# Optimization experiments

Measured on AMD Instinct MI355X. Metric: run time of the kernel, lower is better.

## Reference

```python
import jax, jax.numpy as jnp
import numpy as np

N, E, D_IN, D_OUT = 50000, 600000, 128, 128
BETA, ALPHA = 0.4, 0.6


def setup_inputs() -> dict:
    key = jax.random.key(0)
    ks = jax.random.split(key, 8)
    def xavier(k, shape):
        std = (2.0 / (shape[0] + shape[1])) ** 0.5
        return jax.random.normal(k, shape, jnp.float32) * std
    x = jax.random.normal(ks[0], (N, D_IN), jnp.float32)
    edge_index = jax.random.randint(ks[1], (2, E), 0, N, jnp.int32)
    Wq = xavier(ks[2], (D_IN, D_OUT))
    Wk = xavier(ks[3], (D_IN, D_OUT))
    Wv = xavier(ks[4], (D_IN, D_IN))
    W_gcn = xavier(ks[5], (D_IN, D_IN))   # GCNConv linear weight [out, in]
    b_gcn = jnp.zeros((D_IN,), jnp.float32)
    W_lin = xavier(ks[6], (D_OUT, D_IN))  # nn.Linear weight [out, in]
    b_lin = jnp.zeros((D_OUT,), jnp.float32)
    return {"x": x, "edge_index": edge_index, "Wq": Wq, "Wk": Wk, "Wv": Wv,
            "W_gcn": W_gcn, "b_gcn": b_gcn, "W_lin": W_lin, "b_lin": b_lin}


def gcn_conv(x, edge_index, W, b):
    # PyG GCNConv default: add self-loops, symmetric deg^-1/2 normalization.
    n = x.shape[0]
    loops = jnp.arange(n, dtype=edge_index.dtype)
    src = jnp.concatenate([edge_index[0], loops])
    dst = jnp.concatenate([edge_index[1], loops])
    deg = jax.ops.segment_sum(jnp.ones_like(dst, jnp.float32), dst, num_segments=n)
    d_inv_sqrt = jax.lax.rsqrt(deg)  # deg >= 1 thanks to self-loops
    norm = d_inv_sqrt[src] * d_inv_sqrt[dst]  # [E+N]
    xw = x @ W.T                               # [N, d]
    out = jax.ops.segment_sum(xw[src] * norm[:, None], dst, num_segments=n)
    return out + b


def reference(x, edge_index, Wq, Wk, Wv, W_gcn, b_gcn, W_lin, b_lin):
    n, d_in = x.shape
    q = x @ Wq
    q_hat = q / jnp.linalg.norm(q)  # Frobenius norm
    k = x @ Wk
    k_hat = k / jnp.linalg.norm(k)
    v = x @ Wv
    # qk = q_hat @ (k_hat^T @ 1) / in_channels  -> [n]
    qk = (q_hat @ k_hat.sum(axis=0)) / d_in
    # D = diag(1 + qk); inverse of diagonal is elementwise reciprocal
    scale = 1.0 / (1.0 + qk)
    attn = v + (q_hat @ (k_hat.T @ v)) / d_in  # [n, d_in]
    Z = BETA * scale[:, None] * attn + (1.0 - BETA) * x
    gcn = gcn_conv(x, edge_index, W_gcn, b_gcn)
    # self.dropout(gcn) result is discarded in the source -> no-op
    Z_out = (1.0 - ALPHA) * Z + ALPHA * gcn
    return Z_out @ W_lin.T + b_lin
```

## Files before the change

kernel.cpp:

```cpp
#include <hip/hip_runtime.h>
#include <hip/hip_fp16.h>
#include <cstdint>
#include <cstddef>

#define D 128
#define XTS 72
typedef unsigned short u16;
typedef short bf16x8 __attribute__((ext_vector_type(8)));
typedef float f32x4 __attribute__((ext_vector_type(4)));

__device__ __forceinline__ u16 f2b(float f) {
    uint32_t u = __float_as_uint(f);
    return (u16)((u + 0x7FFFu + ((u >> 16) & 1u)) >> 16);
}
__device__ __forceinline__ float b2f(u16 b) {
    return __uint_as_float(((uint32_t)b) << 16);
}

#define SWZ(r, k) ((k) ^ (((r) & 7) << 3))

__global__ void k_prep(const float* __restrict__ Wv, const float* __restrict__ Wg,
                       const float* __restrict__ bg, const float* __restrict__ Wl,
                       const float* __restrict__ bl,
                       u16* __restrict__ Bcatb, float* __restrict__ biasout)
{
    const int b = blockIdx.x;
    const int t = threadIdx.x;
    if (b < 384) {
        const int strip = b >> 7, n = b & 127;
        float val;
        if (strip == 0) {
            float s = 0.f;
#pragma unroll 8
            for (int m = 0; m < D; ++m) s += Wv[t * D + m] * Wl[n * D + m];
            val = s;
        } else if (strip == 1) {
            val = Wl[n * D + t];
        } else {
            float s = 0.f;
#pragma unroll 8
            for (int m = 0; m < D; ++m) s += Wl[n * D + m] * Wg[m * D + t];
            val = 0.6f * s;
        }
        Bcatb[(size_t)b * D + t] = f2b(val);
    } else {
        float s = 0.f;
#pragma unroll 8
        for (int m = 0; m < D; ++m) s += bg[m] * Wl[t * D + m];
        biasout[t] = bl[t] + 0.6f * s;
    }
}

__global__ void k_init(int* __restrict__ cnt, int M)
{
    const int i = blockIdx.x * 256 + threadIdx.x;
    if (i < M) cnt[i] = 0;
}

__global__ void k_hist(const int* __restrict__ dst, int* __restrict__ cnt,
                       int* __restrict__ epos, int E)
{
    const int e = blockIdx.x * 256 + threadIdx.x;
    if (e < E) epos[e] = atomicAdd(&cnt[dst[e]], 1);
}

__global__ __launch_bounds__(1024) void k_scan1(const int* __restrict__ cnt,
                                                int* __restrict__ offs,
                                                int* __restrict__ bsum,
                                                float* __restrict__ dinv, int M)
{
    __shared__ int wsum[16];
    const int t = threadIdx.x, lane = t & 63, w = t >> 6;
    const int i = blockIdx.x * 1024 + t;
    const int v = (i < M) ? cnt[i] : 0;
    if (i < M) dinv[i] = rsqrtf((float)(v + 1));
    int s = v;
    for (int off = 1; off < 64; off <<= 1) {
        int n = __shfl_up(s, off);
        if (lane >= off) s += n;
    }
    if (lane == 63) wsum[w] = s;
    __syncthreads();
    if (w == 0) {
        int ss = (lane < 16) ? wsum[lane] : 0;
        for (int off = 1; off < 16; off <<= 1) {
            int n = __shfl_up(ss, off);
            if (lane >= off) ss += n;
        }
        if (lane < 16) wsum[lane] = ss;
    }
    __syncthreads();
    const int woff = (w == 0) ? 0 : wsum[w - 1];
    if (i < M) offs[i] = woff + s - v;
    if (t == 1023) bsum[blockIdx.x] = wsum[15];
}

__global__ void k_scanB(int* __restrict__ bsum, int nb)
{
    const int t = threadIdx.x;
    int v = (t < nb) ? bsum[t] : 0;
    int s = v;
    for (int off = 1; off < 64; off <<= 1) {
        int n = __shfl_up(s, off);
        if (t >= off) s += n;
    }
    if (t < nb) bsum[t] = s - v;
}

__global__ void k_scan2(const int* __restrict__ bsum, int* __restrict__ offs, int M)
{
    const int i = blockIdx.x * 256 + threadIdx.x;
    if (i < M) offs[i] += bsum[i >> 10];
}

__global__ void k_fill(const int* __restrict__ src, const int* __restrict__ dst,
                       const int* __restrict__ epos,
                       const float* __restrict__ dinv,
                       const int* __restrict__ offs,
                       uint32_t* __restrict__ cpk, int E)
{
    const int e = blockIdx.x * 256 + threadIdx.x;
    if (e < E) {
        const int s = src[e], d = dst[e];
        const int pos = offs[d] + epos[e];
        const float w = dinv[s] * dinv[d];
        const u16 hb = __half_as_ushort(__float2half(w));
        cpk[pos] = (uint32_t)(u16)s | ((uint32_t)hb << 16);
    }
}

__global__ __launch_bounds__(256) void k_gram(const float* __restrict__ x,
                                              u16* __restrict__ part,
                                              float* __restrict__ pcs, int M)
{
    __shared__ u16 xT[D * XTS];
    const int t = threadIdx.x;
    const int P = (int)gridDim.x;
    const int chunk = (M + P - 1) / P;
    const int rbeg = blockIdx.x * chunk;
    const int rend = min(rbeg + chunk, M);
    const int lane = t & 63, w = t >> 6;
    const int fr = lane & 15, kg = lane >> 4;

    f32x4 acc[2][8] = {};
    float csacc = 0.f;

    for (int r0 = rbeg; r0 < rend; r0 += 64) {
#pragma unroll
        for (int p = 0; p < 8; ++p) {
            const int flat = t + 256 * p;
            const int rr = flat & 63;
            const int c4 = flat >> 6;
            const int gr = r0 + rr;
            float4 v = make_float4(0.f, 0.f, 0.f, 0.f);
            if (gr < rend) v = *(const float4*)(x + (size_t)gr * D + c4 * 4);
            u16* dst = xT + (c4 * 4) * XTS + rr;
            dst[0]       = f2b(v.x);
            dst[XTS]     = f2b(v.y);
            dst[2 * XTS] = f2b(v.z);
            dst[3 * XTS] = f2b(v.w);
        }
        __syncthreads();
#pragma unroll
        for (int ks = 0; ks < 2; ++ks) {
            const int rb = ks * 32 + kg * 8;
            bf16x8 a[2], b[8];
#pragma unroll
            for (int i = 0; i < 2; ++i) {
                const int m = w * 32 + 16 * i + fr;
                a[i] = *(const bf16x8*)(xT + m * XTS + rb);
            }
#pragma unroll
            for (int j = 0; j < 8; ++j) {
                const int n = 16 * j + fr;
                b[j] = *(const bf16x8*)(xT + n * XTS + rb);
            }
#pragma unroll
            for (int i = 0; i < 2; ++i)
#pragma unroll
                for (int j = 0; j < 8; ++j)
                    acc[i][j] = __builtin_amdgcn_mfma_f32_16x16x32_bf16(a[i], b[j], acc[i][j], 0, 0, 0);
        }
        if (t < D) {
            const u16* col = xT + t * XTS;
#pragma unroll 16
            for (int r = 0; r < 64; ++r) csacc += b2f(col[r]);
        }
        __syncthreads();
    }
    u16* pp = part + (size_t)blockIdx.x * (D * D);
#pragma unroll
    for (int i = 0; i < 2; ++i)
#pragma unroll
        for (int reg = 0; reg < 4; ++reg) {
            const int m = w * 32 + 16 * i + kg * 4 + reg;
#pragma unroll
            for (int j = 0; j < 8; ++j)
                pp[(size_t)m * D + 16 * j + fr] = f2b(acc[i][j][reg]);
        }
    if (t < D) pcs[(size_t)blockIdx.x * D + t] = csacc;
}

__global__ void k_redC(const u16* __restrict__ part, float* __restrict__ Craw,
                       const float* __restrict__ pcs, float* __restrict__ csx, int P)
{
    if (blockIdx.x < 64) {
        const int e = blockIdx.x * 256 + threadIdx.x;
        float s0 = 0.f, s1 = 0.f, s2 = 0.f, s3 = 0.f,
              s4 = 0.f, s5 = 0.f, s6 = 0.f, s7 = 0.f;
        int p = 0;
        for (; p + 8 <= P; p += 8) {
            s0 += b2f(part[(size_t)(p + 0) * (D * D) + e]);
            s1 += b2f(part[(size_t)(p + 1) * (D * D) + e]);
            s2 += b2f(part[(size_t)(p + 2) * (D * D) + e]);
            s3 += b2f(part[(size_t)(p + 3) * (D * D) + e]);
            s4 += b2f(part[(size_t)(p + 4) * (D * D) + e]);
            s5 += b2f(part[(size_t)(p + 5) * (D * D) + e]);
            s6 += b2f(part[(size_t)(p + 6) * (D * D) + e]);
            s7 += b2f(part[(size_t)(p + 7) * (D * D) + e]);
        }
        for (; p < P; ++p) s0 += b2f(part[(size_t)p * (D * D) + e]);
        Craw[e] = ((s0 + s1) + (s2 + s3)) + ((s4 + s5) + (s6 + s7));
    } else {
        __shared__ float red[16][16];
        const int pb = blockIdx.x - 64;
        const int cl = threadIdx.x & 15;
        const int sl = threadIdx.x >> 4;
        const int col = pb * 16 + cl;
        float s = 0.f;
#pragma unroll 8
        for (int p = sl; p < P; p += 16) s += pcs[(size_t)p * D + col];
        red[sl][cl] = s;
        __syncthreads();
        if (sl == 0) {
            float tot = 0.f;
#pragma unroll
            for (int i = 0; i < 16; ++i) tot += red[i][cl];
            csx[col] = tot;
        }
    }
}

__device__ __forceinline__ void gemm16x64(const u16* __restrict__ A,
                                          const u16* __restrict__ B,
                                          f32x4 acc[4], int rw, int cw,
                                          int fr, int kg)
{
#pragma unroll
    for (int ks = 0; ks < 4; ++ks) {
        const int kb = ks * 32 + kg * 8;
        const int r = rw + fr;
        const bf16x8 a = *(const bf16x8*)(A + r * D + SWZ(r, kb));
#pragma unroll
        for (int j = 0; j < 4; ++j) {
            const int n = cw + 16 * j + fr;
            const bf16x8 b = *(const bf16x8*)(B + n * D + SWZ(n, kb));
            acc[j] = __builtin_amdgcn_mfma_f32_16x16x32_bf16(a, b, acc[j], 0, 0, 0);
        }
    }
}

__global__ __launch_bounds__(1024) void k_small(const float* __restrict__ Graw,
                                                const float* __restrict__ csx_g,
                                                const float* __restrict__ Wq,
                                                const float* __restrict__ Wk,
                                                const u16* __restrict__ stripV,
                                                float* __restrict__ xkq,
                                                u16* __restrict__ C5b)
{
    __shared__ u16 Ga[D * D];
    __shared__ u16 Bq[D * D];
    __shared__ u16 Bk[D * D];
    __shared__ u16 T2[D * D];
    __shared__ float csx[D];
    __shared__ float ksum[D];
    __shared__ float trsh[32];
    __shared__ float invS;
    const int t = threadIdx.x;
    const int lane = t & 63, w = t >> 6;
    const int fr = lane & 15, kg = lane >> 4;
    const int rw = (w & 7) * 16, cw = (w >> 3) * 64;

    if (t < D) csx[t] = csx_g[t];
#pragma unroll
    for (int p = 0; p < 4; ++p) {
        const int e4 = t + 1024 * p;
        const int e = e4 * 4;
        const int i = e >> 7, m = e & 127;
        const float4 g = *(const float4*)(Graw + e);
        u16 gb[4] = {f2b(g.x), f2b(g.y), f2b(g.z), f2b(g.w)};
        *(uint2*)(Ga + i * D + SWZ(i, m)) = *(const uint2*)gb;
        const float4 q = *(const float4*)(Wq + e);
        const float4 k = *(const float4*)(Wk + e);
        Bq[(m + 0) * D + SWZ(m + 0, i)] = f2b(q.x);
        Bq[(m + 1) * D + SWZ(m + 1, i)] = f2b(q.y);
        Bq[(m + 2) * D + SWZ(m + 2, i)] = f2b(q.z);
        Bq[(m + 3) * D + SWZ(m + 3, i)] = f2b(q.w);
        Bk[(m + 0) * D + SWZ(m + 0, i)] = f2b(k.x);
        Bk[(m + 1) * D + SWZ(m + 1, i)] = f2b(k.y);
        Bk[(m + 2) * D + SWZ(m + 2, i)] = f2b(k.z);
        Bk[(m + 3) * D + SWZ(m + 3, i)] = f2b(k.w);
    }
    __syncthreads();

    {
        f32x4 acc[4] = {};
        gemm16x64(Ga, Bk, acc, rw, cw, fr, kg);
        float tk = 0.f;
#pragma unroll
        for (int reg = 0; reg < 4; ++reg) {
            const int row = rw + kg * 4 + reg;
#pragma unroll
            for (int j = 0; j < 4; ++j) {
                const int col = cw + 16 * j + fr;
                const float h = acc[j][reg];
                T2[col * D + SWZ(col, row)] = f2b(h);
                tk += h * b2f(Bk[col * D + SWZ(col, row)]);
            }
        }
        for (int off = 32; off > 0; off >>= 1) tk += __shfl_down(tk, off);
        if (lane == 0) trsh[w] = tk;
    }
    __syncthreads();
    {
        f32x4 acc[4] = {};
        gemm16x64(Ga, Bq, acc, rw, cw, fr, kg);
        float tq = 0.f;
#pragma unroll
        for (int reg = 0; reg < 4; ++reg) {
            const int row = rw + kg * 4 + reg;
#pragma unroll
            for (int j = 0; j < 4; ++j) {
                const int col = cw + 16 * j + fr;
                tq += acc[j][reg] * b2f(Bq[col * D + SWZ(col, row)]);
            }
        }
        for (int off = 32; off > 0; off >>= 1) tq += __shfl_down(tq, off);
        if (lane == 0) trsh[16 + w] = tq;
    }
    __syncthreads();
    if (t == 0) {
        float sk = 0.f, sq = 0.f;
#pragma unroll
        for (int i = 0; i < 16; ++i) { sk += trsh[i]; sq += trsh[16 + i]; }
        invS = 1.0f / (sqrtf(sq) * sqrtf(sk) * 128.0f);
    }
    if (t < D) {
        float s = 0.f;
#pragma unroll 8
        for (int j = 0; j < D; ++j) s += csx[j] * Wk[j * D + t];
        ksum[t] = s;
    }
#pragma unroll
    for (int p = 0; p < 4; ++p) {
        const int e4 = t + 1024 * p;
        const int e = e4 * 4;
        const int i = e >> 7, m = e & 127;
        const float4 q = *(const float4*)(Wq + e);
        u16 qb[4] = {f2b(q.x), f2b(q.y), f2b(q.z), f2b(q.w)};
        *(uint2*)(Ga + i * D + SWZ(i, m)) = *(const uint2*)qb;
    }
#pragma unroll
    for (int p = 0; p < 2; ++p) {
        const int e8 = (t + 1024 * p) * 8;
        const int n = e8 >> 7, i0 = e8 & 127;
        *(uint4*)(Bq + n * D + SWZ(n, i0)) = *(const uint4*)(stripV + n * D + i0);
    }
    __syncthreads();
    {
        f32x4 acc[4] = {};
        gemm16x64(T2, Bq, acc, rw, cw, fr, kg);
        const float inv = invS;
#pragma unroll
        for (int reg = 0; reg < 4; ++reg) {
            const int m = rw + kg * 4 + reg;
#pragma unroll
            for (int j = 0; j < 4; ++j) {
                const int n = cw + 16 * j + fr;
                Bk[n * D + SWZ(n, m)] = f2b(acc[j][reg] * inv);
            }
        }
    }
    if (t < D) {
        float s = 0.f;
        const float inv = invS;
#pragma unroll 8
        for (int o = 0; o < D; ++o) s += Wq[t * D + o] * ksum[o];
        xkq[t] = s * inv;
    }
    __syncthreads();
    {
        f32x4 acc[4] = {};
        gemm16x64(Ga, Bk, acc, rw, cw, fr, kg);
#pragma unroll
        for (int reg = 0; reg < 4; ++reg) {
            const int r = rw + kg * 4 + reg;
#pragma unroll
            for (int j = 0; j < 4; ++j) {
                const int n = cw + 16 * j + fr;
                C5b[n * D + r] = f2b(b2f(stripV[n * D + r]) + acc[j][reg]);
            }
        }
    }
}

__global__ __launch_bounds__(256) void k_ugemm(const float* __restrict__ x,
                                               const u16* __restrict__ stripU,
                                               u16* __restrict__ ub, int M)
{
    __shared__ u16 As[64 * D];
    __shared__ u16 Bs[64 * D];
    const int t = threadIdx.x;
    const int row0 = blockIdx.x * 64;

#pragma unroll
    for (int p = 0; p < 4; ++p) {
        const int flat = t + 256 * p;
        const int r = flat >> 4, kg = flat & 15;
        int gr = row0 + r; if (gr > M - 1) gr = M - 1;
        const float4 f0 = *(const float4*)(x + (size_t)gr * D + kg * 8);
        const float4 f1 = *(const float4*)(x + (size_t)gr * D + kg * 8 + 4);
        u16 rr[8] = {f2b(f0.x), f2b(f0.y), f2b(f0.z), f2b(f0.w),
                     f2b(f1.x), f2b(f1.y), f2b(f1.z), f2b(f1.w)};
        *(uint4*)(As + r * D + SWZ(r, kg * 8)) = *(const uint4*)rr;
    }
#pragma unroll
    for (int p = 0; p < 4; ++p) {
        const int flat = t + 256 * p;
        const int r = flat >> 4, kg = flat & 15;
        const uint4 v = *(const uint4*)(stripU + (size_t)r * D + kg * 8);
        *(uint4*)(Bs + r * D + SWZ(r, kg * 8)) = v;
    }
    __syncthreads();

    const int lane = t & 63, w = t >> 6;
    const int wr = (w >> 1) * 32, wc = (w & 1) * 32;
    const int fr = lane & 15, kg2 = lane >> 4;

#pragma unroll
    for (int h = 0; h < 2; ++h) {
        f32x4 acc[2][2] = {};
#pragma unroll
        for (int ks = 0; ks < 4; ++ks) {
            const int kb = ks * 32 + kg2 * 8;
            bf16x8 a[2], b[2];
#pragma unroll
            for (int i = 0; i < 2; ++i) {
                const int r = wr + 16 * i + fr;
                a[i] = *(const bf16x8*)(As + r * D + SWZ(r, kb));
            }
#pragma unroll
            for (int j = 0; j < 2; ++j) {
                const int r = wc + 16 * j + fr;
                b[j] = *(const bf16x8*)(Bs + r * D + SWZ(r, kb));
            }
#pragma unroll
            for (int i = 0; i < 2; ++i)
#pragma unroll
                for (int j = 0; j < 2; ++j)
                    acc[i][j] = __builtin_amdgcn_mfma_f32_16x16x32_bf16(a[i], b[j], acc[i][j], 0, 0, 0);
        }
        __syncthreads();
        if (h == 0) {
#pragma unroll
            for (int p = 0; p < 4; ++p) {
                const int flat = t + 256 * p;
                const int r = flat >> 4, kg = flat & 15;
                const uint4 v = *(const uint4*)(stripU + (size_t)(64 + r) * D + kg * 8);
                *(uint4*)(Bs + r * D + SWZ(r, kg * 8)) = v;
            }
        }
        const int col0 = h * 64;
#pragma unroll
        for (int i = 0; i < 2; ++i) {
#pragma unroll
            for (int reg = 0; reg < 4; ++reg) {
                const int r = row0 + wr + 16 * i + kg2 * 4 + reg;
                if (r < M) {
#pragma unroll
                    for (int j = 0; j < 2; ++j) {
                        const int col = col0 + wc + 16 * j + fr;
                        ub[(size_t)r * D + col] = f2b(acc[i][j][reg]);
                    }
                }
            }
        }
        if (h == 0) __syncthreads();
    }
}

__global__ __launch_bounds__(256) void k_final(const float* __restrict__ x,
                                               const u16* __restrict__ C5b,
                                               const u16* __restrict__ stripL,
                                               const u16* __restrict__ ub,
                                               const int* __restrict__ cnt,
                                               const float* __restrict__ xkq,
                                               const float* __restrict__ biasout,
                                               float* __restrict__ out, int M)
{
    __shared__ u16 As[64 * D];
    __shared__ u16 Bs[64 * D];
    __shared__ float scaleS[64];
    const int t = threadIdx.x;
    const int row0 = blockIdx.x * 64;
    const int half = blockIdx.y;

#pragma unroll
    for (int p = 0; p < 4; ++p) {
        const int flat = t + 256 * p;
        const int r = flat >> 4, kg = flat & 15;
        int gr = row0 + r; if (gr > M - 1) gr = M - 1;
        const float4 f0 = *(const float4*)(x + (size_t)gr * D + kg * 8);
        const float4 f1 = *(const float4*)(x + (size_t)gr * D + kg * 8 + 4);
        u16 rr[8] = {f2b(f0.x), f2b(f0.y), f2b(f0.z), f2b(f0.w),
                     f2b(f1.x), f2b(f1.y), f2b(f1.z), f2b(f1.w)};
        *(uint4*)(As + r * D + SWZ(r, kg * 8)) = *(const uint4*)rr;
    }
#pragma unroll
    for (int p = 0; p < 4; ++p) {
        const int flat = t + 256 * p;
        const int r = flat >> 4, kg = flat & 15;
        const uint4 v = *(const uint4*)(C5b + (size_t)(half * 64 + r) * D + kg * 8);
        *(uint4*)(Bs + r * D + SWZ(r, kg * 8)) = v;
    }
    __syncthreads();

    {
        const int rr = t >> 2, qq = t & 3;
        float s = 0.f;
#pragma unroll
        for (int i = 0; i < 4; ++i) {
            const int kk = qq * 32 + i * 8;
            const bf16x8 a = *(const bf16x8*)(As + rr * D + SWZ(rr, kk));
            const u16* ap = (const u16*)&a;
#pragma unroll
            for (int jj = 0; jj < 8; ++jj) s += b2f(ap[jj]) * xkq[kk + jj];
        }
        s += __shfl_xor(s, 1);
        s += __shfl_xor(s, 2);
        if (qq == 0) scaleS[rr] = 0.16f / (1.0f + s);
    }

    const int lane = t & 63, w = t >> 6;
    const int wr = (w >> 1) * 32, wc = (w & 1) * 32;
    const int fr = lane & 15, kg2 = lane >> 4;

    f32x4 acc1[2][2] = {};
#pragma unroll
    for (int ks = 0; ks < 4; ++ks) {
        const int kb = ks * 32 + kg2 * 8;
        bf16x8 a[2], b[2];
#pragma unroll
        for (int i = 0; i < 2; ++i) {
            const int r = wr + 16 * i + fr;
            a[i] = *(const bf16x8*)(As + r * D + SWZ(r, kb));
        }
#pragma unroll
        for (int j = 0; j < 2; ++j) {
            const int r = wc + 16 * j + fr;
            b[j] = *(const bf16x8*)(Bs + r * D + SWZ(r, kb));
        }
#pragma unroll
        for (int i = 0; i < 2; ++i)
#pragma unroll
            for (int j = 0; j < 2; ++j)
                acc1[i][j] = __builtin_amdgcn_mfma_f32_16x16x32_bf16(a[i], b[j], acc1[i][j], 0, 0, 0);
    }
    __syncthreads();
#pragma unroll
    for (int p = 0; p < 4; ++p) {
        const int flat = t + 256 * p;
        const int r = flat >> 4, kg = flat & 15;
        const uint4 v = *(const uint4*)(stripL + (size_t)(half * 64 + r) * D + kg * 8);
        *(uint4*)(Bs + r * D + SWZ(r, kg * 8)) = v;
    }
    __syncthreads();

    f32x4 acc2[2][2] = {};
#pragma unroll
    for (int ks = 0; ks < 4; ++ks) {
        const int kb = ks * 32 + kg2 * 8;
        bf16x8 a[2], b[2];
#pragma unroll
        for (int i = 0; i < 2; ++i) {
            const int r = wr + 16 * i + fr;
            a[i] = *(const bf16x8*)(As + r * D + SWZ(r, kb));
        }
#pragma unroll
        for (int j = 0; j < 2; ++j) {
            const int r = wc + 16 * j + fr;
            b[j] = *(const bf16x8*)(Bs + r * D + SWZ(r, kb));
        }
#pragma unroll
        for (int i = 0; i < 2; ++i)
#pragma unroll
            for (int j = 0; j < 2; ++j)
                acc2[i][j] = __builtin_amdgcn_mfma_f32_16x16x32_bf16(a[i], b[j], acc2[i][j], 0, 0, 0);
    }

#pragma unroll
    for (int i = 0; i < 2; ++i) {
#pragma unroll
        for (int reg = 0; reg < 4; ++reg) {
            const int rloc = wr + 16 * i + kg2 * 4 + reg;
            const int r = row0 + rloc;
            if (r < M) {
                const float rc = scaleS[rloc];
                const float sc = 1.0f / (float)(cnt[r] + 1);
#pragma unroll
                for (int j = 0; j < 2; ++j) {
                    const int c = half * 64 + wc + 16 * j + fr;
                    const size_t idx = (size_t)r * D + c;
                    out[idx] = rc * acc1[i][j][reg] + 0.24f * acc2[i][j][reg]
                             + biasout[c] + sc * b2f(ub[idx]);
                }
            }
        }
    }
}

__global__ __launch_bounds__(256) void k_gather(const int* __restrict__ offs,
                                                const int* __restrict__ cnt,
                                                const uint32_t* __restrict__ cpk,
                                                const u16* __restrict__ ub,
                                                float* __restrict__ out, int M)
{
    const int t = threadIdx.x;
    const int w = t >> 6, lane = t & 63;
    const int d = blockIdx.x * 4 + w;
    if (d >= M) return;
    const int g = lane >> 4, sub = lane & 15;
    const int beg = offs[d];
    const int n = cnt[d];
    if (n == 0) return;
    const int end = beg + n;
    float acc[8] = {};
    for (int j0 = beg; j0 < end; j0 += 16) {
        int ss[4]; float ww[4];
#pragma unroll
        for (int q = 0; q < 4; ++q) {
            const int j = j0 + 4 * q + g;
            int s = 0; float wv = 0.f;
            if (j < end) {
                const uint32_t p = cpk[j];
                s = (int)(p & 0xFFFFu);
                wv = __half2float(__ushort_as_half((u16)(p >> 16)));
            }
            ss[q] = s; ww[q] = wv;
        }
        uint4 rr[4];
#pragma unroll
        for (int q = 0; q < 4; ++q)
            rr[q] = *(const uint4*)(ub + (size_t)ss[q] * D + sub * 8);
#pragma unroll
        for (int q = 0; q < 4; ++q) {
            const u16* p = (const u16*)&rr[q];
            const float wv = ww[q];
#pragma unroll
            for (int i = 0; i < 8; ++i) acc[i] += wv * b2f(p[i]);
        }
    }
#pragma unroll
    for (int i = 0; i < 8; ++i) {
        acc[i] += __shfl_xor(acc[i], 16);
        acc[i] += __shfl_xor(acc[i], 32);
    }
    if (g == 0) {
        float* o = out + (size_t)d * D + sub * 8;
        float4 o0 = *(float4*)o, o1 = *(float4*)(o + 4);
        o0.x += acc[0]; o0.y += acc[1]; o0.z += acc[2]; o0.w += acc[3];
        o1.x += acc[4]; o1.y += acc[5]; o1.z += acc[6]; o1.w += acc[7];
        *(float4*)o = o0; *(float4*)(o + 4) = o1;
    }
}

extern "C" void kernel_launch(void* const* d_in, const int* in_sizes, int n_in,
                              void* d_out, int out_size, void* d_ws, size_t ws_size,
                              hipStream_t stream)
{
    const float* x  = (const float*)d_in[0];
    const int*   ei = (const int*)d_in[1];
    const float* Wq = (const float*)d_in[2];
    const float* Wk = (const float*)d_in[3];
    const float* Wv = (const float*)d_in[4];
    const float* Wg = (const float*)d_in[5];
    const float* bg = (const float*)d_in[6];
    const float* Wl = (const float*)d_in[7];
    const float* bl = (const float*)d_in[8];

    const int M = in_sizes[0] / D;
    const int E = in_sizes[1] / 2;
    const size_t NQ = (size_t)M * D;
    const int P = 512;
    const int NBG = (M + 63) / 64;
    const int NB = (M + 1023) / 1024;

    char* base = (char*)d_ws;
    auto alloc = [&](size_t bytes) -> char* {
        char* p = base; base += (bytes + 63) & ~(size_t)63; return p;
    };
    u16*   part    = (u16*)alloc((size_t)P * D * D * 2);
    float* Graw    = (float*)alloc(D * D * 4);
    float* pcs     = (float*)alloc((size_t)P * D * 4);
    float* csx     = (float*)alloc(D * 4);
    float* dinv    = (float*)alloc((size_t)M * 4);
    float* xkq     = (float*)alloc(D * 4);
    float* biasout = (float*)alloc(D * 4);
    int*   cnt     = (int*)alloc((size_t)M * 4);
    int*   offs    = (int*)alloc((size_t)M * 4);
    int*   bsum    = (int*)alloc(64 * 4);
    int*   epos    = (int*)alloc((size_t)E * 4);
    uint32_t* cpk  = (uint32_t*)alloc((size_t)E * 4);
    u16*   Bcatb   = (u16*)alloc((size_t)384 * D * 2);
    u16*   C5b     = (u16*)alloc(D * D * 2);
    u16*   ub      = (u16*)alloc(NQ * 2);

    const u16* stripV = Bcatb;
    const u16* stripL = Bcatb + D * D;
    const u16* stripU = Bcatb + 2 * D * D;

    float* out = (float*)d_out;

    k_prep<<<dim3(385), dim3(128), 0, stream>>>(Wv, Wg, bg, Wl, bl, Bcatb, biasout);
    k_init<<<(M + 255) / 256, 256, 0, stream>>>(cnt, M);
    k_hist<<<(E + 255) / 256, 256, 0, stream>>>(ei + E, cnt, epos, E);
    k_scan1<<<NB, 1024, 0, stream>>>(cnt, offs, bsum, dinv, M);
    k_scanB<<<1, 64, 0, stream>>>(bsum, NB);
    k_scan2<<<(M + 255) / 256, 256, 0, stream>>>(bsum, offs, M);
    k_fill<<<(E + 255) / 256, 256, 0, stream>>>(ei, ei + E, epos, dinv, offs, cpk, E);

    k_gram<<<P, 256, 0, stream>>>(x, part, pcs, M);
    k_redC<<<72, 256, 0, stream>>>(part, Graw, pcs, csx, P);
    k_small<<<1, 1024, 0, stream>>>(Graw, csx, Wq, Wk, stripV, xkq, C5b);
    k_ugemm<<<NBG, 256, 0, stream>>>(x, stripU, ub, M);
    k_final<<<dim3(NBG, 2), 256, 0, stream>>>(x, C5b, stripL, ub, cnt, xkq, biasout, out, M);
    k_gather<<<(M + 3) / 4, 256, 0, stream>>>(offs, cnt, cpk, ub, out, M);
}
```

Baseline: 186.0 us.

## Fuse ugemm into final dense kernel and fold scan carry into consumers

Merges the U-projection GEMM into the final dense kernel, so each (row-block, half) block computes its 64-column slice of ub, writes it, and uses it directly instead of reading ub back from global memory. The block-level scan carry is now computed redundantly in each k_fill and k_gather block from bsum, which removes the k_scanB and k_scan2 launches. Zeroing of cnt and bsum is folded into k_prep, removing k_init. The result is four fewer kernel launches and one fewer round trip of ub through global memory. The cost is a small per-block 64-wide shuffle scan, and bsum must be zeroed so that unused entries beyond the real block count read as zero.

```diff
diff --git a/kernel.cpp b/kernel.cpp
--- a/kernel.cpp
+++ b/kernel.cpp
@@ -22,7 +22,8 @@
 __global__ void k_prep(const float* __restrict__ Wv, const float* __restrict__ Wg,
                        const float* __restrict__ bg, const float* __restrict__ Wl,
                        const float* __restrict__ bl,
-                       u16* __restrict__ Bcatb, float* __restrict__ biasout)
+                       u16* __restrict__ Bcatb, float* __restrict__ biasout,
+                       int* __restrict__ cnt, int* __restrict__ bsum, int M)
 {
     const int b = blockIdx.x;
     const int t = threadIdx.x;
@@ -43,18 +44,16 @@
             val = 0.6f * s;
         }
         Bcatb[(size_t)b * D + t] = f2b(val);
-    } else {
+    } else if (b == 384) {
         float s = 0.f;
 #pragma unroll 8
         for (int m = 0; m < D; ++m) s += bg[m] * Wl[t * D + m];
         biasout[t] = bl[t] + 0.6f * s;
-    }
-}
-
-__global__ void k_init(int* __restrict__ cnt, int M)
-{
-    const int i = blockIdx.x * 256 + threadIdx.x;
-    if (i < M) cnt[i] = 0;
+        if (t < 64) bsum[t] = 0;
+    } else {
+        const int i = (b - 385) * 128 + t;
+        if (i < M) cnt[i] = 0;
+    }
 }
 
 __global__ void k_hist(const int* __restrict__ dst, int* __restrict__ cnt,
@@ -95,34 +94,29 @@
     if (t == 1023) bsum[blockIdx.x] = wsum[15];
 }
 
-__global__ void k_scanB(int* __restrict__ bsum, int nb)
-{
-    const int t = threadIdx.x;
-    int v = (t < nb) ? bsum[t] : 0;
-    int s = v;
-    for (int off = 1; off < 64; off <<= 1) {
-        int n = __shfl_up(s, off);
-        if (t >= off) s += n;
-    }
-    if (t < nb) bsum[t] = s - v;
-}
-
-__global__ void k_scan2(const int* __restrict__ bsum, int* __restrict__ offs, int M)
-{
-    const int i = blockIdx.x * 256 + threadIdx.x;
-    if (i < M) offs[i] += bsum[i >> 10];
-}
-
 __global__ void k_fill(const int* __restrict__ src, const int* __restrict__ dst,
                        const int* __restrict__ epos,
                        const float* __restrict__ dinv,
                        const int* __restrict__ offs,
+                       const int* __restrict__ bsum,
                        uint32_t* __restrict__ cpk, int E)
 {
-    const int e = blockIdx.x * 256 + threadIdx.x;
+    __shared__ int sbcar[64];
+    const int t = threadIdx.x;
+    if (t < 64) {
+        const int v = bsum[t];
+        int s = v;
+        for (int off = 1; off < 64; off <<= 1) {
+            int n = __shfl_up(s, off);
+            if (t >= off) s += n;
+        }
+        sbcar[t] = s - v;
+    }
+    __syncthreads();
+    const int e = blockIdx.x * 256 + t;
     if (e < E) {
         const int s = src[e], d = dst[e];
-        const int pos = offs[d] + epos[e];
+        const int pos = sbcar[d >> 10] + offs[d] + epos[e];
         const float w = dinv[s] * dinv[d];
         const u16 hb = __half_as_ushort(__float2half(w));
         cpk[pos] = (uint32_t)(u16)s | ((uint32_t)hb << 16);
@@ -404,14 +398,22 @@
     }
 }
 
-__global__ __launch_bounds__(256) void k_ugemm(const float* __restrict__ x,
+__global__ __launch_bounds__(256) void k_dense(const float* __restrict__ x,
                                                const u16* __restrict__ stripU,
-                                               u16* __restrict__ ub, int M)
+                                               const u16* __restrict__ C5b,
+                                               const u16* __restrict__ stripL,
+                                               const int* __restrict__ cnt,
+                                               const float* __restrict__ xkq,
+                                               const float* __restrict__ biasout,
+                                               u16* __restrict__ ub,
+                                               float* __restrict__ out, int M)
 {
     __shared__ u16 As[64 * D];
     __shared__ u16 Bs[64 * D];
+    __shared__ float scaleS[64];
     const int t = threadIdx.x;
     const int row0 = blockIdx.x * 64;
+    const int half = blockIdx.y;
 
 #pragma unroll
     for (int p = 0; p < 4; ++p) {
@@ -428,94 +430,53 @@
     for (int p = 0; p < 4; ++p) {
         const int flat = t + 256 * p;
         const int r = flat >> 4, kg = flat & 15;
-        const uint4 v = *(const uint4*)(stripU + (size_t)r * D + kg * 8);
+        const uint4 v = *(const uint4*)(stripU + (size_t)(half * 64 + r) * D + kg * 8);
         *(uint4*)(Bs + r * D + SWZ(r, kg * 8)) = v;
     }
     __syncthreads();
+
+    {
+        const int rr = t >> 2, qq = t & 3;
+        float s = 0.f;
+#pragma unroll
+        for (int i = 0; i < 4; ++i) {
+            const int kk = qq * 32 + i * 8;
+            const bf16x8 a = *(const bf16x8*)(As + rr * D + SWZ(rr, kk));
+            const u16* ap = (const u16*)&a;
+#pragma unroll
+            for (int jj = 0; jj < 8; ++jj) s += b2f(ap[jj]) * xkq[kk + jj];
+        }
+        s += __shfl_xor(s, 1);
+        s += __shfl_xor(s, 2);
+        if (qq == 0) scaleS[rr] = 0.16f / (1.0f + s);
+    }
 
     const int lane = t & 63, w = t >> 6;
     const int wr = (w >> 1) * 32, wc = (w & 1) * 32;
     const int fr = lane & 15, kg2 = lane >> 4;
 
-#pragma unroll
-    for (int h = 0; h < 2; ++h) {
-        f32x4 acc[2][2] = {};
-#pragma unroll
-        for (int ks = 0; ks < 4; ++ks) {
-            const int kb = ks * 32 + kg2 * 8;
-            bf16x8 a[2], b[2];
-#pragma unroll
-            for (int i = 0; i < 2; ++i) {
-                const int r = wr + 16 * i + fr;
-                a[i] = *(const bf16x8*)(As + r * D + SWZ(r, kb));
-            }
-#pragma unroll
-            for (int j = 0; j < 2; ++j) {
-                const int r = wc + 16 * j + fr;
-                b[j] = *(const bf16x8*)(Bs + r * D + SWZ(r, kb));
-            }
-#pragma unroll
-            for (int i = 0; i < 2; ++i)
-#pragma unroll
-                for (int j = 0; j < 2; ++j)
-                    acc[i][j] = __builtin_amdgcn_mfma_f32_16x16x32_bf16(a[i], b[j], acc[i][j], 0, 0, 0);
-        }
-        __syncthreads();
-        if (h == 0) {
-#pragma unroll
-            for (int p = 0; p < 4; ++p) {
-                const int flat = t + 256 * p;
-                const int r = flat >> 4, kg = flat & 15;
-                const uint4 v = *(const uint4*)(stripU + (size_t)(64 + r) * D + kg * 8);
-                *(uint4*)(Bs + r * D + SWZ(r, kg * 8)) = v;
-            }
-        }
-        const int col0 = h * 64;
+    f32x4 accU[2][2] = {};
+#pragma unroll
+    for (int ks = 0; ks < 4; ++ks) {
+        const int kb = ks * 32 + kg2 * 8;
+        bf16x8 a[2], b[2];
 #pragma unroll
         for (int i = 0; i < 2; ++i) {
-#pragma unroll
-            for (int reg = 0; reg < 4; ++reg) {
-                const int r = row0 + wr + 16 * i + kg2 * 4 + reg;
-                if (r < M) {
-#pragma unroll
-                    for (int j = 0; j < 2; ++j) {
-                        const int col = col0 + wc + 16 * j + fr;
-                        ub[(size_t)r * D + col] = f2b(acc[i][j][reg]);
-                    }
-                }
-            }
-        }
-        if (h == 0) __syncthreads();
-    }
-}
-
-__global__ __launch_bounds__(256) void k_final(const float* __restrict__ x,
-                                               const u16* __restrict__ C5b,
-                                               const u16* __restrict__ stripL,
-                                               const u16* __restrict__ ub,
-                                               const int* __restrict__ cnt,
-                                               const float* __restrict__ xkq,
-                                               const float* __restrict__ biasout,
-                                               float* __restrict__ out, int M)
-{
-    __shared__ u16 As[64 * D];
-    __shared__ u16 Bs[64 * D];
-    __shared__ float scaleS[64];
-    const int t = threadIdx.x;
-    const int row0 = blockIdx.x * 64;
-    const int half = blockIdx.y;
-
-#pragma unroll
-    for (int p = 0; p < 4; ++p) {
-        const int flat = t + 256 * p;
-        const int r = flat >> 4, kg = flat & 15;
-        int gr = row0 + r; if (gr > M - 1) gr = M - 1;
-        const float4 f0 = *(const float4*)(x + (size_t)gr * D + kg * 8);
-        const float4 f1 = *(const float4*)(x + (size_t)gr * D + kg * 8 + 4);
-        u16 rr[8] = {f2b(f0.x), f2b(f0.y), f2b(f0.z), f2b(f0.w),
-                     f2b(f1.x), f2b(f1.y), f2b(f1.z), f2b(f1.w)};
-        *(uint4*)(As + r * D + SWZ(r, kg * 8)) = *(const uint4*)rr;
-    }
+            const int r = wr + 16 * i + fr;
+            a[i] = *(const bf16x8*)(As + r * D + SWZ(r, kb));
+        }
+#pragma unroll
+        for (int j = 0; j < 2; ++j) {
+            const int r = wc + 16 * j + fr;
+            b[j] = *(const bf16x8*)(Bs + r * D + SWZ(r, kb));
+        }
+#pragma unroll
+        for (int i = 0; i < 2; ++i)
+#pragma unroll
+            for (int j = 0; j < 2; ++j)
+                accU[i][j] = __builtin_amdgcn_mfma_f32_16x16x32_bf16(a[i], b[j], accU[i][j], 0, 0, 0);
+    }
+    __syncthreads();
 #pragma unroll
     for (int p = 0; p < 4; ++p) {
         const int flat = t + 256 * p;
@@ -524,26 +485,6 @@
         *(uint4*)(Bs + r * D + SWZ(r, kg * 8)) = v;
     }
     __syncthreads();
-
-    {
-        const int rr = t >> 2, qq = t & 3;
-        float s = 0.f;
-#pragma unroll
-        for (int i = 0; i < 4; ++i) {
-            const int kk = qq * 32 + i * 8;
-            const bf16x8 a = *(const bf16x8*)(As + rr * D + SWZ(rr, kk));
-            const u16* ap = (const u16*)&a;
-#pragma unroll
-            for (int jj = 0; jj < 8; ++jj) s += b2f(ap[jj]) * xkq[kk + jj];
-        }
-        s += __shfl_xor(s, 1);
-        s += __shfl_xor(s, 2);
-        if (qq == 0) scaleS[rr] = 0.16f / (1.0f + s);
-    }
-
-    const int lane = t & 63, w = t >> 6;
-    const int wr = (w >> 1) * 32, wc = (w & 1) * 32;
-    const int fr = lane & 15, kg2 = lane >> 4;
 
     f32x4 acc1[2][2] = {};
 #pragma unroll
@@ -611,8 +552,10 @@
                 for (int j = 0; j < 2; ++j) {
                     const int c = half * 64 + wc + 16 * j + fr;
                     const size_t idx = (size_t)r * D + c;
+                    const float uv = accU[i][j][reg];
+                    ub[idx] = f2b(uv);
                     out[idx] = rc * acc1[i][j][reg] + 0.24f * acc2[i][j][reg]
-                             + biasout[c] + sc * b2f(ub[idx]);
+                             + biasout[c] + sc * uv;
                 }
             }
         }
@@ -621,18 +564,30 @@
 
 __global__ __launch_bounds__(256) void k_gather(const int* __restrict__ offs,
                                                 const int* __restrict__ cnt,
+                                                const int* __restrict__ bsum,
                                                 const uint32_t* __restrict__ cpk,
                                                 const u16* __restrict__ ub,
                                                 float* __restrict__ out, int M)
 {
+    __shared__ int sbcar[64];
     const int t = threadIdx.x;
+    if (t < 64) {
+        const int v = bsum[t];
+        int s = v;
+        for (int off = 1; off < 64; off <<= 1) {
+            int n = __shfl_up(s, off);
+            if (t >= off) s += n;
+        }
+        sbcar[t] = s - v;
+    }
+    __syncthreads();
     const int w = t >> 6, lane = t & 63;
     const int d = blockIdx.x * 4 + w;
     if (d >= M) return;
     const int g = lane >> 4, sub = lane & 15;
-    const int beg = offs[d];
     const int n = cnt[d];
     if (n == 0) return;
+    const int beg = sbcar[d >> 10] + offs[d];
     const int end = beg + n;
     float acc[8] = {};
     for (int j0 = beg; j0 < end; j0 += 16) {
@@ -693,7 +648,6 @@
     const size_t NQ = (size_t)M * D;
     const int P = 512;
     const int NBG = (M + 63) / 64;
-    const int NB = (M + 1023) / 1024;
 
     char* base = (char*)d_ws;
     auto alloc = [&](size_t bytes) -> char* {
@@ -721,18 +675,15 @@
 
     float* out = (float*)d_out;
 
-    k_prep<<<dim3(385), dim3(128), 0, stream>>>(Wv, Wg, bg, Wl, bl, Bcatb, biasout);
-    k_init<<<(M + 255) / 256, 256, 0, stream>>>(cnt, M);
+    k_prep<<<dim3(385 + (M + 127) / 128), dim3(128), 0, stream>>>(Wv, Wg, bg, Wl, bl,
+                                                                  Bcatb, biasout, cnt, bsum, M);
     k_hist<<<(E + 255) / 256, 256, 0, stream>>>(ei + E, cnt, epos, E);
-    k_scan1<<<NB, 1024, 0, stream>>>(cnt, offs, bsum, dinv, M);
-    k_scanB<<<1, 64, 0, stream>>>(bsum, NB);
-    k_scan2<<<(M + 255) / 256, 256, 0, stream>>>(bsum, offs, M);
-    k_fill<<<(E + 255) / 256, 256, 0, stream>>>(ei, ei + E, epos, dinv, offs, cpk, E);
+    k_scan1<<<(M + 1023) / 1024, 1024, 0, stream>>>(cnt, offs, bsum, dinv, M);
+    k_fill<<<(E + 255) / 256, 256, 0, stream>>>(ei, ei + E, epos, dinv, offs, bsum, cpk, E);
 
     k_gram<<<P, 256, 0, stream>>>(x, part, pcs, M);
     k_redC<<<72, 256, 0, stream>>>(part, Graw, pcs, csx, P);
     k_small<<<1, 1024, 0, stream>>>(Graw, csx, Wq, Wk, stripV, xkq, C5b);
-    k_ugemm<<<NBG, 256, 0, stream>>>(x, stripU, ub, M);
-    k_final<<<dim3(NBG, 2), 256, 0, stream>>>(x, C5b, stripL, ub, cnt, xkq, biasout, out, M);
-    k_gather<<<(M + 3) / 4, 256, 0, stream>>>(offs, cnt, cpk, ub, out, M);
-}
+    k_dense<<<dim3(NBG, 2), 256, 0, stream>>>(x, stripU, C5b, stripL, cnt, xkq, biasout, ub, out, M);
+    k_gather<<<(M + 3) / 4, 256, 0, stream>>>(offs, cnt, bsum, cpk, ub, out, M);
+}
```

Result: faster. 176.3 us (-5.2%).
